# Kernel optimization log

Hardware: AMD Instinct MI355X
Metric: run time of the kernel (lower is better)

## Reference

```python
import jax, jax.numpy as jnp
import numpy as np

N = 8192
D = 128
NUM_CLASSES = 16
EPS = 1e-8  # torch cosine_similarity eps


def setup_inputs() -> dict:
    key = jax.random.key(0)
    k1, k2 = jax.random.split(key)
    inp = jax.random.normal(k1, (N, D), dtype=jnp.float32)
    targets = jax.random.randint(k2, (N,), 0, NUM_CLASSES, dtype=jnp.int64)
    temperature = jnp.asarray(0.5, dtype=jnp.float32)
    return {"input": inp, "targets": targets, "temperature": temperature}


def reference(input, targets, temperature):
    # clamp temperature to [0.1, 1.0] as the module does in forward
    temp = jnp.clip(temperature, 0.1, 1.0)

    # cosine similarity matrix [N, N]
    norms = jnp.maximum(jnp.linalg.norm(input, axis=1, keepdims=True), EPS)
    xn = input / norms
    sim = jnp.matmul(xn, xn.T) / temp          # [N, N]
    E = jnp.exp(sim)                            # [N, N]

    same = targets[:, None] == targets[None, :]  # [N, N] bool
    diag = jnp.diagonal(E)                       # exp(s_ii)
    pos = jnp.sum(jnp.where(same, E, 0.0), axis=1) - diag   # same-class, excl self
    tot = jnp.sum(E, axis=1) - diag                          # pos + neg
    per_sample_loss = -jnp.log(pos / tot)                    # [N]

    # per-class aggregation (segment sums with static num_segments)
    counts = jax.ops.segment_sum(jnp.ones_like(per_sample_loss), targets,
                                 num_segments=NUM_CLASSES)
    sums = jax.ops.segment_sum(per_sample_loss, targets,
                               num_segments=NUM_CLASSES)
    safe_counts = jnp.maximum(counts, 1.0)
    class_mean = sums / safe_counts

    # class weights: (1/count) normalized over present classes
    inv = jnp.where(counts > 0, 1.0 / safe_counts, 0.0)
    weights = inv / jnp.sum(inv)

    # only classes with more than one sample contribute
    valid = counts > 1
    weighted = jnp.where(valid, class_mean * weights, 0.0)
    n_valid = jnp.sum(valid.astype(jnp.float32))
    loss = jnp.sum(weighted) / n_valid
    return loss
```

## Files before the change

kernel.cpp:

```cpp
#include <hip/hip_runtime.h>

#define N 8192
#define D 128
#define NCLS 16
#define SLOT 512
#define RSTRIDE 256

typedef unsigned short u16;
typedef __attribute__((ext_vector_type(8))) short v8s;
typedef __attribute__((ext_vector_type(16))) float f32x16;

static __device__ inline u16 f2bf(float f) {
  unsigned int u = __builtin_bit_cast(unsigned int, f);
  unsigned int r = u + 0x7fffu + ((u >> 16) & 1u);
  return (u16)(r >> 16);
}

__global__ __launch_bounds__(256) void k_norm(float* __restrict__ buf,
                                              const float* __restrict__ temp) {
  int wave = threadIdx.x >> 6;
  int lane = threadIdx.x & 63;
  int row = blockIdx.x * 4 + wave;
  const float* p = buf + (size_t)row * D + lane * 2;
  float x = p[0], y = p[1];
  float ss = x * x + y * y;
#pragma unroll
  for (int m = 32; m >= 1; m >>= 1) ss += __shfl_xor(ss, m);
  float t = fminf(fmaxf(temp[0], 0.1f), 1.0f);
  float sc = sqrtf(1.4426950408889634f / t);
  float inv = sc / fmaxf(sqrtf(ss), 1e-8f);
  unsigned int u0 = (unsigned int)f2bf(x * inv);
  unsigned int u1 = (unsigned int)f2bf(y * inv);
  reinterpret_cast<unsigned int*>(buf)[(size_t)row * 128 + lane] = u0 | (u1 << 16);
}

__global__ __launch_bounds__(256) void k_sim(float* __restrict__ buf,
                                             const int* __restrict__ tgt) {
  __shared__ __align__(16) char lds[2][32 * 256];

  const int tid = threadIdx.x;
  const int wave = tid >> 6;
  const int lane = tid & 63;
  const int l31 = lane & 31;
  const int h = lane >> 5;
  const int lm = l31 & 15;

  const u16* xnb = reinterpret_cast<const u16*>(buf);

  const int rowstrip = blockIdx.x >> 5;
  const int cq = blockIdx.x & 31;
  const int rwb = rowstrip * 128 + wave * 32;
  const int colblock = cq * 256;

  v8s afrag[8];
  {
    const u16* ap = xnb + (size_t)(rwb + l31) * RSTRIDE + h * 8;
#pragma unroll
    for (int kk = 0; kk < 8; ++kk)
      afrag[kk] = *reinterpret_cast<const v8s*>(ap + kk * 16);
  }

  int trow[16];
#pragma unroll
  for (int r = 0; r < 16; ++r)
    trow[r] = tgt[rwb + ((r & 3) + 8 * (r >> 2) + 4 * h)];

  float tot_acc[16], pos_acc[16];
#pragma unroll
  for (int r = 0; r < 16; ++r) { tot_acc[r] = 0.f; pos_acc[r] = 0.f; }

  auto stage = [&](int g, int bsel) {
    int rowbase = colblock + g * 32;
#pragma unroll
    for (int i = 0; i < 2; ++i) {
      int L = i * 256 + tid;
      int row = L >> 4;
      int s = (L & 15) ^ (row & 15);
      const char* src = reinterpret_cast<const char*>(buf) +
                        (size_t)(rowbase + row) * SLOT + s * 16;
      char* dst = &lds[bsel][(i * 256 + wave * 64) * 16];
      __builtin_amdgcn_global_load_lds(
          (const __attribute__((address_space(1))) void*)src,
          (__attribute__((address_space(3))) void*)dst, 16, 0, 0);
    }
  };

  stage(0, 0);
  __syncthreads();

  const int lbase = l31 * 256;

  for (int g = 0; g < 8; ++g) {
    int cur = g & 1;
    if (g + 1 < 8) stage(g + 1, cur ^ 1);

    int c0 = colblock + g * 32;
    int tcol = tgt[c0 + l31];

    f32x16 acc;
#pragma unroll
    for (int r = 0; r < 16; ++r) acc[r] = 0.f;
    const char* lb = lds[cur];
#pragma unroll
    for (int kk = 0; kk < 8; ++kk) {
      v8s bf = *reinterpret_cast<const v8s*>(lb + lbase + (((2 * kk + h) ^ lm) << 4));
      acc = __builtin_amdgcn_mfma_f32_32x32x16_bf16(afrag[kk], bf, acc, 0, 0, 0);
    }

    if (c0 != rwb) {
#pragma unroll
      for (int r = 0; r < 16; ++r) {
        float e = exp2f(acc[r]);
        tot_acc[r] += e;
        pos_acc[r] += (tcol == trow[r]) ? e : 0.f;
      }
    } else {
#pragma unroll
      for (int r = 0; r < 16; ++r) {
        float e = exp2f(acc[r]);
        if (l31 == ((r & 3) + 8 * (r >> 2) + 4 * h)) e = 0.f;
        tot_acc[r] += e;
        pos_acc[r] += (tcol == trow[r]) ? e : 0.f;
      }
    }
    __syncthreads();
  }

#pragma unroll
  for (int r = 0; r < 16; ++r) {
    float p = pos_acc[r], q = tot_acc[r];
#pragma unroll
    for (int m = 1; m <= 16; m <<= 1) {
      p += __shfl_xor(p, m);
      q += __shfl_xor(q, m);
    }
    if (l31 == 0) {
      int row = rwb + ((r & 3) + 8 * (r >> 2) + 4 * h);
      float* slot = reinterpret_cast<float*>(
          reinterpret_cast<char*>(buf) + (size_t)row * SLOT + 256);
      slot[cq] = p;
      slot[32 + cq] = q;
    }
  }
}

__global__ __launch_bounds__(128) void k_tail_a(float* __restrict__ buf,
                                                const int* __restrict__ tgt) {
  __shared__ float cs[NCLS], cc[NCLS];
  int tid = threadIdx.x;
  if (tid < NCLS) { cs[tid] = 0.f; cc[tid] = 0.f; }
  __syncthreads();
  int row = blockIdx.x * 128 + tid;
  const float4* s4 = reinterpret_cast<const float4*>(
      reinterpret_cast<const char*>(buf) + (size_t)row * SLOT + 256);
  float pos = 0.f, tot = 0.f;
#pragma unroll
  for (int i = 0; i < 8; ++i) {
    float4 a = s4[i], b = s4[8 + i];
    pos += a.x + a.y + a.z + a.w;
    tot += b.x + b.y + b.z + b.w;
  }
  float loss = logf(tot) - logf(pos);
  int c = tgt[row];
  atomicAdd(&cs[c], loss);
  atomicAdd(&cc[c], 1.0f);
  __syncthreads();
  if (tid < 2 * NCLS) {
    float* dst = reinterpret_cast<float*>(
        reinterpret_cast<char*>(buf) + (size_t)blockIdx.x * SLOT);
    dst[tid] = (tid < NCLS) ? cs[tid] : cc[tid - NCLS];
  }
}

__global__ __launch_bounds__(1024) void k_final(const float* __restrict__ buf,
                                                float* __restrict__ out) {
  __shared__ float cs[NCLS], cc[NCLS];
  int tid = threadIdx.x;
  if (tid < NCLS) { cs[tid] = 0.f; cc[tid] = 0.f; }
  __syncthreads();
  {
    int b = tid >> 4, c = tid & 15;
    const float* src = reinterpret_cast<const float*>(
        reinterpret_cast<const char*>(buf) + (size_t)b * SLOT);
    atomicAdd(&cs[c], src[c]);
    atomicAdd(&cc[c], src[NCLS + c]);
  }
  __syncthreads();
  if (tid < 64) {
    int c = tid;
    float s = 0.f, n = 0.f;
    if (c < NCLS) { s = cs[c]; n = cc[c]; }
    float safe = fmaxf(n, 1.0f);
    float mean = s / safe;
    float inv = (n > 0.5f) ? 1.0f / safe : 0.f;
    float valid = (n > 1.5f) ? 1.f : 0.f;
    float w = (n > 1.5f) ? mean * inv : 0.f;
    float sinv = inv, sw = w, sv = valid;
#pragma unroll
    for (int m = 1; m <= 32; m <<= 1) {
      sinv += __shfl_xor(sinv, m);
      sw += __shfl_xor(sw, m);
      sv += __shfl_xor(sv, m);
    }
    if (c == 0) out[0] = sw / sinv / sv;
  }
}

extern "C" void kernel_launch(void* const* d_in, const int* in_sizes, int n_in,
                              void* d_out, int out_size, void* d_ws, size_t ws_size,
                              hipStream_t stream) {
  float* buf = (float*)d_in[0];
  const int* tgt = (const int*)d_in[1];
  const float* temp = (const float*)d_in[2];
  float* out = (float*)d_out;
  (void)d_ws; (void)ws_size;

  k_norm<<<N / 4, 256, 0, stream>>>(buf, temp);
  k_sim<<<2048, 256, 0, stream>>>(buf, tgt);
  k_tail_a<<<64, 128, 0, stream>>>(buf, tgt);
  k_final<<<1, 1024, 0, stream>>>(buf, out);
}
```

Baseline: 112.6 us.

## Use native exp/log, atomic row accumulation, fused tail kernel, unrolled stage loop

Replaces exp2f with the raw v_exp_f32 instruction in the similarity epilogue and logf with v_log_f32 in the tail. Per-row partial sums are now accumulated with global float atomics into a slot that k_norm zeroes, instead of 32 per-column-block slots. The two tail kernels are merged into one single-block kernel, removing a launch. The staging address math is hoisted and the tile loop fully unrolled. The trade-off is global atomic contention (32 adds per row slot) and a serial single-block tail over 8192 rows.

```diff
diff --git a/kernel.cpp b/kernel.cpp
--- a/kernel.cpp
+++ b/kernel.cpp
@@ -14,6 +14,17 @@
   unsigned int u = __builtin_bit_cast(unsigned int, f);
   unsigned int r = u + 0x7fffu + ((u >> 16) & 1u);
   return (u16)(r >> 16);
+}
+
+static __device__ inline float fast_exp2(float x) {
+  float r;
+  asm("v_exp_f32 %0, %1" : "=v"(r) : "v"(x));
+  return r;
+}
+static __device__ inline float fast_log2(float x) {
+  float r;
+  asm("v_log_f32 %0, %1" : "=v"(r) : "v"(x));
+  return r;
 }
 
 __global__ __launch_bounds__(256) void k_norm(float* __restrict__ buf,
@@ -32,6 +43,10 @@
   unsigned int u0 = (unsigned int)f2bf(x * inv);
   unsigned int u1 = (unsigned int)f2bf(y * inv);
   reinterpret_cast<unsigned int*>(buf)[(size_t)row * 128 + lane] = u0 | (u1 << 16);
+  if (lane == 0) {
+    float2 z; z.x = 0.f; z.y = 0.f;
+    *reinterpret_cast<float2*>(reinterpret_cast<char*>(buf) + (size_t)row * SLOT + 256) = z;
+  }
 }
 
 __global__ __launch_bounds__(256) void k_sim(float* __restrict__ buf,
@@ -69,15 +84,19 @@
 #pragma unroll
   for (int r = 0; r < 16; ++r) { tot_acc[r] = 0.f; pos_acc[r] = 0.f; }
 
+  const char* srcb[2];
+#pragma unroll
+  for (int i = 0; i < 2; ++i) {
+    int L = i * 256 + tid;
+    int row = L >> 4;
+    int s = (L & 15) ^ (row & 15);
+    srcb[i] = reinterpret_cast<const char*>(buf) + (size_t)(colblock + row) * SLOT + s * 16;
+  }
+
   auto stage = [&](int g, int bsel) {
-    int rowbase = colblock + g * 32;
 #pragma unroll
     for (int i = 0; i < 2; ++i) {
-      int L = i * 256 + tid;
-      int row = L >> 4;
-      int s = (L & 15) ^ (row & 15);
-      const char* src = reinterpret_cast<const char*>(buf) +
-                        (size_t)(rowbase + row) * SLOT + s * 16;
+      const char* src = srcb[i] + g * 32 * SLOT;
       char* dst = &lds[bsel][(i * 256 + wave * 64) * 16];
       __builtin_amdgcn_global_load_lds(
           (const __attribute__((address_space(1))) void*)src,
@@ -90,6 +109,7 @@
 
   const int lbase = l31 * 256;
 
+#pragma unroll
   for (int g = 0; g < 8; ++g) {
     int cur = g & 1;
     if (g + 1 < 8) stage(g + 1, cur ^ 1);
@@ -110,14 +130,14 @@
     if (c0 != rwb) {
 #pragma unroll
       for (int r = 0; r < 16; ++r) {
-        float e = exp2f(acc[r]);
+        float e = fast_exp2(acc[r]);
         tot_acc[r] += e;
         pos_acc[r] += (tcol == trow[r]) ? e : 0.f;
       }
     } else {
 #pragma unroll
       for (int r = 0; r < 16; ++r) {
-        float e = exp2f(acc[r]);
+        float e = fast_exp2(acc[r]);
         if (l31 == ((r & 3) + 8 * (r >> 2) + 4 * h)) e = 0.f;
         tot_acc[r] += e;
         pos_acc[r] += (tcol == trow[r]) ? e : 0.f;
@@ -138,64 +158,50 @@
       int row = rwb + ((r & 3) + 8 * (r >> 2) + 4 * h);
       float* slot = reinterpret_cast<float*>(
           reinterpret_cast<char*>(buf) + (size_t)row * SLOT + 256);
-      slot[cq] = p;
-      slot[32 + cq] = q;
-    }
-  }
-}
-
-__global__ __launch_bounds__(128) void k_tail_a(float* __restrict__ buf,
-                                                const int* __restrict__ tgt) {
-  __shared__ float cs[NCLS], cc[NCLS];
+      atomicAdd(&slot[0], p);
+      atomicAdd(&slot[1], q);
+    }
+  }
+}
+
+__global__ __launch_bounds__(1024) void k_tail(const float* __restrict__ buf,
+                                               const int* __restrict__ tgt,
+                                               float* __restrict__ out) {
+  __shared__ float cs[16][NCLS], cc[16][NCLS];
   int tid = threadIdx.x;
-  if (tid < NCLS) { cs[tid] = 0.f; cc[tid] = 0.f; }
-  __syncthreads();
-  int row = blockIdx.x * 128 + tid;
-  const float4* s4 = reinterpret_cast<const float4*>(
-      reinterpret_cast<const char*>(buf) + (size_t)row * SLOT + 256);
-  float pos = 0.f, tot = 0.f;
-#pragma unroll
-  for (int i = 0; i < 8; ++i) {
-    float4 a = s4[i], b = s4[8 + i];
-    pos += a.x + a.y + a.z + a.w;
-    tot += b.x + b.y + b.z + b.w;
-  }
-  float loss = logf(tot) - logf(pos);
-  int c = tgt[row];
-  atomicAdd(&cs[c], loss);
-  atomicAdd(&cc[c], 1.0f);
-  __syncthreads();
-  if (tid < 2 * NCLS) {
-    float* dst = reinterpret_cast<float*>(
-        reinterpret_cast<char*>(buf) + (size_t)blockIdx.x * SLOT);
-    dst[tid] = (tid < NCLS) ? cs[tid] : cc[tid - NCLS];
-  }
-}
-
-__global__ __launch_bounds__(1024) void k_final(const float* __restrict__ buf,
-                                                float* __restrict__ out) {
-  __shared__ float cs[NCLS], cc[NCLS];
-  int tid = threadIdx.x;
-  if (tid < NCLS) { cs[tid] = 0.f; cc[tid] = 0.f; }
-  __syncthreads();
-  {
-    int b = tid >> 4, c = tid & 15;
-    const float* src = reinterpret_cast<const float*>(
-        reinterpret_cast<const char*>(buf) + (size_t)b * SLOT);
-    atomicAdd(&cs[c], src[c]);
-    atomicAdd(&cc[c], src[NCLS + c]);
+  int w = tid >> 6;
+  if ((tid & 63) < NCLS) { cs[w][tid & 63] = 0.f; cc[w][tid & 63] = 0.f; }
+  __syncthreads();
+#pragma unroll
+  for (int j = 0; j < 8; ++j) {
+    int row = j * 1024 + tid;
+    const float* slot = reinterpret_cast<const float*>(
+        reinterpret_cast<const char*>(buf) + (size_t)row * SLOT + 256);
+    float pos = slot[0], tot = slot[1];
+    float loss = 0.69314718055994531f * (fast_log2(tot) - fast_log2(pos));
+    int c = tgt[row];
+    atomicAdd(&cs[w][c], loss);
+    atomicAdd(&cc[w][c], 1.0f);
+  }
+  __syncthreads();
+  if (tid < NCLS) {
+    float s = 0.f, n = 0.f;
+#pragma unroll
+    for (int w2 = 0; w2 < 16; ++w2) { s += cs[w2][tid]; n += cc[w2][tid]; }
+    cs[0][tid] = s;
+    cc[0][tid] = n;
   }
   __syncthreads();
   if (tid < 64) {
     int c = tid;
     float s = 0.f, n = 0.f;
-    if (c < NCLS) { s = cs[c]; n = cc[c]; }
+    if (c < NCLS) { s = cs[0][c]; n = cc[0][c]; }
     float safe = fmaxf(n, 1.0f);
     float mean = s / safe;
     float inv = (n > 0.5f) ? 1.0f / safe : 0.f;
     float valid = (n > 1.5f) ? 1.f : 0.f;
-    float w = (n > 1.5f) ? mean * inv : 0.f;
-    float sinv = inv, sw = w, sv = valid;
+    float wgt = (n > 1.5f) ? mean * inv : 0.f;
+    float sinv = inv, sw = wgt, sv = valid;
 #pragma unroll
     for (int m = 1; m <= 32; m <<= 1) {
       sinv += __shfl_xor(sinv, m);
@@ -217,6 +223,5 @@
 
   k_norm<<<N / 4, 256, 0, stream>>>(buf, temp);
   k_sim<<<2048, 256, 0, stream>>>(buf, tgt);
-  k_tail_a<<<64, 128, 0, stream>>>(buf, tgt);
-  k_final<<<1, 1024, 0, stream>>>(buf, out);
-}
+  k_tail<<<1, 1024, 0, stream>>>(buf, tgt, out);
+}
```

After: 140.7 us. 24.9% more time.
